# Kernel tuning notes

Hardware: AMD Instinct MI355X
Metric: run time of the kernel (lower is better)

## Reference

```python
import jax, jax.numpy as jnp
import numpy as np

EMBED_DIM = 384
NUM_HEADS = 6
HEAD_DIM = EMBED_DIM // NUM_HEADS
SCALE = HEAD_DIM ** -0.5


def setup_inputs() -> dict:
    key = jax.random.key(0)
    k1, k2 = jax.random.split(key)
    b, n, q, hw, c = 8, 5, 15, 196, EMBED_DIM
    k = 5  # shots
    x_query = jax.random.normal(k1, (b, n, q, hw, c), dtype=jnp.float32)
    x_support = jax.random.normal(k2, (b, n, k, c), dtype=jnp.float32)
    return {"x_query": x_query, "x_support": x_support}


def reference(x_query, x_support):
    b, n, k, c = x_support.shape
    _, _, q, hw, _ = x_query.shape
    h, d = NUM_HEADS, HEAD_DIM
    M = n * k            # support tokens
    P = n * q            # query images
    # support tokens as per-head queries: (b, M, h, d)
    qs = x_support.reshape(b, M, h, d)
    # query patch tokens as per-head keys/values: (b, P, hw, h, d)
    kv = x_query.reshape(b, P, hw, h, d)
    # broadcast single support-query block across all P key/value blocks
    # attn: (b, P, h, M, hw)
    attn = jnp.einsum('bmhd,bpwhd->bphmw', qs, kv) * SCALE
    attn = jax.nn.softmax(attn, axis=-1)
    # o: (b, P, M, h, d) -> (b, P, M, c)
    o_query = jnp.einsum('bphmw,bpwhd->bpmhd', attn, kv).reshape(b, P, M, c)
    o_support = x_support.reshape(b, 1, M, c)
    return (o_query, o_support)
```

## Files before the change

### kernel.cpp

```cpp
#include <hip/hip_runtime.h>
#include <stdint.h>

#define HW   196
#define CC   384
#define HH   6
#define DD   64
#define MM   25
#define PP   75
#define BB   8
#define NT   512

#define KTW  113
#define SCW  113

#define OQ_SIZE (BB * PP * MM * CC)

typedef float  f32x4 __attribute__((ext_vector_type(4)));
typedef short  s16x8 __attribute__((ext_vector_type(8)));
union Frag { uint32_t u[4]; s16x8 v; };

__device__ __forceinline__ float bflo(uint32_t u) { return __uint_as_float(u << 16); }
__device__ __forceinline__ float bfhi(uint32_t u) { return __uint_as_float(u & 0xffff0000u); }
__device__ __forceinline__ uint32_t pk_bf16(float a, float b) {
    union { __bf16 h[2]; uint32_t u; } r;
    r.h[0] = (__bf16)a; r.h[1] = (__bf16)b;
    return r.u;
}
__device__ __forceinline__ uint16_t bf16_1(float a) {
    union { __bf16 h; uint16_t u; } r; r.h = (__bf16)a; return r.u;
}

__global__ __launch_bounds__(NT, 8) void attn_kernel(
    const float* __restrict__ xq,
    const float* __restrict__ xs,
    float* __restrict__ out,
    float* __restrict__ out_sup)
{
    __shared__ uint32_t kvT[64 * KTW];
    __shared__ uint32_t scb[MM * SCW];

    const int bid  = blockIdx.x;
    const int h    = bid % HH;
    const int bp   = bid / HH;
    const int b    = bp / PP;
    const int tid  = threadIdx.x;
    const int lane = tid & 63;
    const int wv   = tid >> 6;
    const int lm   = lane & 15;
    const int quad = lane >> 4;

    if (bid < 600 && tid < 16) {
        int idx = bid * 16 + tid;
        ((float4*)out_sup)[idx * 2]     = ((const float4*)xs)[idx * 2];
        ((float4*)out_sup)[idx * 2 + 1] = ((const float4*)xs)[idx * 2 + 1];
    }

    kvT[(tid >> 3) * KTW + 104 + (tid & 7)] = 0;
    if (tid < 200) scb[(tid >> 3) * SCW + 104 + (tid & 7)] = 0;

    Frag afr[2][2];
    #pragma unroll
    for (int mt = 0; mt < 2; mt++) {
        int row = 16 * mt + lm;
        if (row >= MM) row = MM - 1;
        #pragma unroll
        for (int ks = 0; ks < 2; ks++) {
            const float* p = xs + (size_t)b * (MM * CC) + row * CC + h * DD + ks * 32 + quad * 8;
            float4 v0 = *(const float4*)p;
            float4 v1 = *(const float4*)(p + 4);
            afr[mt][ks].u[0] = pk_bf16(v0.x * 0.125f, v0.y * 0.125f);
            afr[mt][ks].u[1] = pk_bf16(v0.z * 0.125f, v0.w * 0.125f);
            afr[mt][ks].u[2] = pk_bf16(v1.x * 0.125f, v1.y * 0.125f);
            afr[mt][ks].u[3] = pk_bf16(v1.z * 0.125f, v1.w * 0.125f);
        }
    }

    {
        uint16_t* scbh = (uint16_t*)scb;
        uint16_t* kvh  = (uint16_t*)kvT;
        const float* slab = xq + (size_t)bp * (HW * CC) + h * DD;
        for (int nt = wv; nt < 13; nt += 8) {
            const int w = 16 * nt + lm;
            float4 v[2][2];
            if (w < HW) {
                const float* p = slab + (size_t)w * CC + quad * 8;
                #pragma unroll
                for (int ks = 0; ks < 2; ks++) {
                    v[ks][0] = *(const float4*)(p + ks * 32);
                    v[ks][1] = *(const float4*)(p + ks * 32 + 4);
                }
            } else {
                #pragma unroll
                for (int ks = 0; ks < 2; ks++) {
                    v[ks][0].x = v[ks][0].y = v[ks][0].z = v[ks][0].w = 0.f;
                    v[ks][1].x = v[ks][1].y = v[ks][1].z = v[ks][1].w = 0.f;
                }
            }
            Frag bf[2];
            #pragma unroll
            for (int ks = 0; ks < 2; ks++) {
                bf[ks].u[0] = pk_bf16(v[ks][0].x, v[ks][0].y);
                bf[ks].u[1] = pk_bf16(v[ks][0].z, v[ks][0].w);
                bf[ks].u[2] = pk_bf16(v[ks][1].x, v[ks][1].y);
                bf[ks].u[3] = pk_bf16(v[ks][1].z, v[ks][1].w);
            }
            f32x4 acc0 = {0.f, 0.f, 0.f, 0.f};
            f32x4 acc1 = {0.f, 0.f, 0.f, 0.f};
            #pragma unroll
            for (int ks = 0; ks < 2; ks++) {
                acc0 = __builtin_amdgcn_mfma_f32_16x16x32_bf16(afr[0][ks].v, bf[ks].v, acc0, 0, 0, 0);
                acc1 = __builtin_amdgcn_mfma_f32_16x16x32_bf16(afr[1][ks].v, bf[ks].v, acc1, 0, 0, 0);
            }
            #pragma unroll
            for (int ks = 0; ks < 2; ks++) {
                #pragma unroll
                for (int c = 0; c < 4; c++) {
                    int d = 32 * ks + 8 * quad + 2 * c;
                    kvh[d * (2 * KTW) + w]       = (uint16_t)(bf[ks].u[c] & 0xffffu);
                    kvh[(d + 1) * (2 * KTW) + w] = (uint16_t)(bf[ks].u[c] >> 16);
                }
            }
            #pragma unroll
            for (int i = 0; i < 4; i++) {
                scbh[(quad * 4 + i) * (2 * SCW) + w] = bf16_1(acc0[i]);
                int r1 = 16 + quad * 4 + i;
                if (r1 < MM) scbh[r1 * (2 * SCW) + w] = bf16_1(acc1[i]);
            }
        }
    }
    __syncthreads();

    {
        const int mt  = wv >> 2;
        const int nt2 = wv & 3;
        int arow = 16 * mt + lm;
        if (arow >= MM) arow = MM - 1;
        f32x4 acc = {0.f, 0.f, 0.f, 0.f};
        float lsum = 0.f;
        #pragma unroll
        for (int ks = 0; ks < 7; ks++) {
            Frag a, e, bfr;
            int abase = arow * SCW + ks * 16 + quad * 4;
            a.u[0] = scb[abase + 0];
            a.u[1] = scb[abase + 1];
            a.u[2] = scb[abase + 2];
            a.u[3] = scb[abase + 3];
            #pragma unroll
            for (int c = 0; c < 4; c++) {
                float e0 = __expf(bflo(a.u[c]));
                float e1 = __expf(bfhi(a.u[c]));
                lsum += e0 + e1;
                e.u[c] = pk_bf16(e0, e1);
            }
            int bbase = (16 * nt2 + lm) * KTW + ks * 16 + quad * 4;
            bfr.u[0] = kvT[bbase + 0];
            bfr.u[1] = kvT[bbase + 1];
            bfr.u[2] = kvT[bbase + 2];
            bfr.u[3] = kvT[bbase + 3];
            acc = __builtin_amdgcn_mfma_f32_16x16x32_bf16(e.v, bfr.v, acc, 0, 0, 0);
        }
        lsum -= (quad == 0) ? 4.0f : 8.0f;
        lsum += __shfl_xor(lsum, 16, 64);
        lsum += __shfl_xor(lsum, 32, 64);
        float* ob = out + (size_t)bp * (MM * CC) + h * DD + 16 * nt2 + lm;
        #pragma unroll
        for (int i = 0; i < 4; i++) {
            int m = 16 * mt + quad * 4 + i;
            float s_i = __shfl(lsum, quad * 4 + i, 64);
            float inv = __builtin_amdgcn_rcpf(s_i);
            if (m < MM) ob[(size_t)m * CC] = acc[i] * inv;
        }
    }
}

extern "C" void kernel_launch(void* const* d_in, const int* in_sizes, int n_in,
                              void* d_out, int out_size, void* d_ws, size_t ws_size,
                              hipStream_t stream) {
    const float* xq = (const float*)d_in[0];
    const float* xs = (const float*)d_in[1];
    float* out = (float*)d_out;
    float* out_sup = out + (size_t)OQ_SIZE;
    attn_kernel<<<BB * PP * HH, NT, 0, stream>>>(xq, xs, out, out_sup);
}
```

Before: 258.3 us.

## Make attention kernel persistent with double-buffered LDS and prefetched KV loads

Replaces one block per (b,p,h) tile with a persistent grid of 512 blocks, each processing a contiguous range of tiles. The next tile's K/V slab is loaded into registers while the current tile's softmax-times-V MFMA runs, and shared buffers are double-buffered so only one barrier per tile is needed. The aim is to hide global load latency behind compute and cut launch and prologue overhead. In exchange, LDS use doubles, occupancy is lowered to 4 blocks per CU, and each block works through its tiles serially, which may leave the machine underfilled.

```diff
diff --git a/kernel.cpp b/kernel.cpp
--- a/kernel.cpp
+++ b/kernel.cpp
@@ -9,6 +9,10 @@
 #define PP   75
 #define BB   8
 #define NT   512
+#define GRID 512
+#define NTILE (BB * PP * HH)
+#define QT   (NTILE / GRID)
+#define RT   (NTILE % GRID)
 
 #define KTW  113
 #define SCW  113
@@ -30,145 +34,186 @@
     union { __bf16 h; uint16_t u; } r; r.h = (__bf16)a; return r.u;
 }
 
-__global__ __launch_bounds__(NT, 8) void attn_kernel(
+__global__ __launch_bounds__(NT, 4) void attn_kernel(
     const float* __restrict__ xq,
     const float* __restrict__ xs,
     float* __restrict__ out,
     float* __restrict__ out_sup)
 {
-    __shared__ uint32_t kvT[64 * KTW];
-    __shared__ uint32_t scb[MM * SCW];
-
-    const int bid  = blockIdx.x;
-    const int h    = bid % HH;
-    const int bp   = bid / HH;
-    const int b    = bp / PP;
+    __shared__ uint32_t kvT[2][64 * KTW];
+    __shared__ uint32_t scb[2][MM * SCW];
+
+    const int blk  = blockIdx.x;
     const int tid  = threadIdx.x;
     const int lane = tid & 63;
     const int wv   = tid >> 6;
     const int lm   = lane & 15;
     const int quad = lane >> 4;
 
-    if (bid < 600 && tid < 16) {
-        int idx = bid * 16 + tid;
-        ((float4*)out_sup)[idx * 2]     = ((const float4*)xs)[idx * 2];
-        ((float4*)out_sup)[idx * 2 + 1] = ((const float4*)xs)[idx * 2 + 1];
-    }
-
-    kvT[(tid >> 3) * KTW + 104 + (tid & 7)] = 0;
-    if (tid < 200) scb[(tid >> 3) * SCW + 104 + (tid & 7)] = 0;
-
-    Frag afr[2][2];
-    #pragma unroll
-    for (int mt = 0; mt < 2; mt++) {
-        int row = 16 * mt + lm;
-        if (row >= MM) row = MM - 1;
+    {
+        int g = blk * NT + tid;
+        if (g < (BB * MM * CC) / 4)
+            ((float4*)out_sup)[g] = ((const float4*)xs)[g];
+    }
+    {
+        int r = tid >> 3, c = tid & 7;
+        kvT[0][r * KTW + 104 + c] = 0;
+        kvT[1][r * KTW + 104 + c] = 0;
+        if (tid < 200) {
+            scb[0][r * SCW + 104 + c] = 0;
+            scb[1][r * SCW + 104 + c] = 0;
+        }
+    }
+
+    const int start = blk * QT + (blk < RT ? blk : RT);
+    const int cnt   = QT + (blk < RT ? 1 : 0);
+
+    const int  w0   = 16 * wv + lm;
+    const int  w1   = 16 * (wv + 8) + lm;
+    const bool has1 = (wv < 5);
+
+    float4 kv0[4], kv1[4];
+
+    auto LOADKV = [&](float4* r, const float* slab, int w, bool act) {
+        if (act && w < HW) {
+            const float* p = slab + (size_t)w * CC + quad * 8;
+            r[0] = *(const float4*)(p);
+            r[1] = *(const float4*)(p + 4);
+            r[2] = *(const float4*)(p + 32);
+            r[3] = *(const float4*)(p + 36);
+        } else {
+            r[0] = r[1] = r[2] = r[3] = make_float4(0.f, 0.f, 0.f, 0.f);
+        }
+    };
+
+    {
+        const int bid = start;
+        const float* slab = xq + (size_t)(bid / HH) * (HW * CC) + (bid % HH) * DD;
+        LOADKV(kv0, slab, w0, true);
+        LOADKV(kv1, slab, w1, has1);
+    }
+
+    for (int i = 0; i < cnt; ++i) {
+        const int cur = i & 1;
+        const int bid = start + i;
+        const int h   = bid % HH;
+        const int bp  = bid / HH;
+        const int b   = bp / PP;
+        uint32_t* kvTc = kvT[cur];
+        uint32_t* scbc = scb[cur];
+
+        float4 ar[2][2][2];
         #pragma unroll
-        for (int ks = 0; ks < 2; ks++) {
-            const float* p = xs + (size_t)b * (MM * CC) + row * CC + h * DD + ks * 32 + quad * 8;
-            float4 v0 = *(const float4*)p;
-            float4 v1 = *(const float4*)(p + 4);
-            afr[mt][ks].u[0] = pk_bf16(v0.x * 0.125f, v0.y * 0.125f);
-            afr[mt][ks].u[1] = pk_bf16(v0.z * 0.125f, v0.w * 0.125f);
-            afr[mt][ks].u[2] = pk_bf16(v1.x * 0.125f, v1.y * 0.125f);
-            afr[mt][ks].u[3] = pk_bf16(v1.z * 0.125f, v1.w * 0.125f);
-        }
-    }
-
-    {
-        uint16_t* scbh = (uint16_t*)scb;
-        uint16_t* kvh  = (uint16_t*)kvT;
-        const float* slab = xq + (size_t)bp * (HW * CC) + h * DD;
-        for (int nt = wv; nt < 13; nt += 8) {
-            const int w = 16 * nt + lm;
-            float4 v[2][2];
-            if (w < HW) {
-                const float* p = slab + (size_t)w * CC + quad * 8;
-                #pragma unroll
-                for (int ks = 0; ks < 2; ks++) {
-                    v[ks][0] = *(const float4*)(p + ks * 32);
-                    v[ks][1] = *(const float4*)(p + ks * 32 + 4);
-                }
-            } else {
-                #pragma unroll
-                for (int ks = 0; ks < 2; ks++) {
-                    v[ks][0].x = v[ks][0].y = v[ks][0].z = v[ks][0].w = 0.f;
-                    v[ks][1].x = v[ks][1].y = v[ks][1].z = v[ks][1].w = 0.f;
-                }
-            }
-            Frag bf[2];
-            #pragma unroll
-            for (int ks = 0; ks < 2; ks++) {
-                bf[ks].u[0] = pk_bf16(v[ks][0].x, v[ks][0].y);
-                bf[ks].u[1] = pk_bf16(v[ks][0].z, v[ks][0].w);
-                bf[ks].u[2] = pk_bf16(v[ks][1].x, v[ks][1].y);
-                bf[ks].u[3] = pk_bf16(v[ks][1].z, v[ks][1].w);
-            }
+        for (int mt = 0; mt < 2; ++mt) {
+            int row = 16 * mt + lm;
+            if (row >= MM) row = MM - 1;
+            const float* p = xs + (size_t)b * (MM * CC) + row * CC + h * DD + quad * 8;
+            #pragma unroll
+            for (int ks = 0; ks < 2; ++ks) {
+                ar[mt][ks][0] = *(const float4*)(p + ks * 32);
+                ar[mt][ks][1] = *(const float4*)(p + ks * 32 + 4);
+            }
+        }
+
+        Frag b00, b01, b10, b11;
+        b00.u[0] = pk_bf16(kv0[0].x, kv0[0].y); b00.u[1] = pk_bf16(kv0[0].z, kv0[0].w);
+        b00.u[2] = pk_bf16(kv0[1].x, kv0[1].y); b00.u[3] = pk_bf16(kv0[1].z, kv0[1].w);
+        b01.u[0] = pk_bf16(kv0[2].x, kv0[2].y); b01.u[1] = pk_bf16(kv0[2].z, kv0[2].w);
+        b01.u[2] = pk_bf16(kv0[3].x, kv0[3].y); b01.u[3] = pk_bf16(kv0[3].z, kv0[3].w);
+        b10.u[0] = pk_bf16(kv1[0].x, kv1[0].y); b10.u[1] = pk_bf16(kv1[0].z, kv1[0].w);
+        b10.u[2] = pk_bf16(kv1[1].x, kv1[1].y); b10.u[3] = pk_bf16(kv1[1].z, kv1[1].w);
+        b11.u[0] = pk_bf16(kv1[2].x, kv1[2].y); b11.u[1] = pk_bf16(kv1[2].z, kv1[2].w);
+        b11.u[2] = pk_bf16(kv1[3].x, kv1[3].y); b11.u[3] = pk_bf16(kv1[3].z, kv1[3].w);
+
+        Frag afr[2][2];
+        #pragma unroll
+        for (int mt = 0; mt < 2; ++mt)
+            #pragma unroll
+            for (int ks = 0; ks < 2; ++ks) {
+                afr[mt][ks].u[0] = pk_bf16(ar[mt][ks][0].x * 0.125f, ar[mt][ks][0].y * 0.125f);
+                afr[mt][ks].u[1] = pk_bf16(ar[mt][ks][0].z * 0.125f, ar[mt][ks][0].w * 0.125f);
+                afr[mt][ks].u[2] = pk_bf16(ar[mt][ks][1].x * 0.125f, ar[mt][ks][1].y * 0.125f);
+                afr[mt][ks].u[3] = pk_bf16(ar[mt][ks][1].z * 0.125f, ar[mt][ks][1].w * 0.125f);
+            }
+
+        uint16_t* kvh = (uint16_t*)kvTc;
+        uint16_t* sch = (uint16_t*)scbc;
+
+        auto P1 = [&](const Frag& f0, const Frag& f1, int w) {
             f32x4 acc0 = {0.f, 0.f, 0.f, 0.f};
             f32x4 acc1 = {0.f, 0.f, 0.f, 0.f};
-            #pragma unroll
-            for (int ks = 0; ks < 2; ks++) {
-                acc0 = __builtin_amdgcn_mfma_f32_16x16x32_bf16(afr[0][ks].v, bf[ks].v, acc0, 0, 0, 0);
-                acc1 = __builtin_amdgcn_mfma_f32_16x16x32_bf16(afr[1][ks].v, bf[ks].v, acc1, 0, 0, 0);
-            }
-            #pragma unroll
-            for (int ks = 0; ks < 2; ks++) {
+            acc0 = __builtin_amdgcn_mfma_f32_16x16x32_bf16(afr[0][0].v, f0.v, acc0, 0, 0, 0);
+            acc1 = __builtin_amdgcn_mfma_f32_16x16x32_bf16(afr[1][0].v, f0.v, acc1, 0, 0, 0);
+            acc0 = __builtin_amdgcn_mfma_f32_16x16x32_bf16(afr[0][1].v, f1.v, acc0, 0, 0, 0);
+            acc1 = __builtin_amdgcn_mfma_f32_16x16x32_bf16(afr[1][1].v, f1.v, acc1, 0, 0, 0);
+            #pragma unroll
+            for (int c = 0; c < 4; ++c) {
+                int d0 = 8 * quad + 2 * c;
+                kvh[d0 * (2 * KTW) + w]          = (uint16_t)(f0.u[c] & 0xffffu);
+                kvh[(d0 + 1) * (2 * KTW) + w]    = (uint16_t)(f0.u[c] >> 16);
+                kvh[(32 + d0) * (2 * KTW) + w]   = (uint16_t)(f1.u[c] & 0xffffu);
+                kvh[(33 + d0) * (2 * KTW) + w]   = (uint16_t)(f1.u[c] >> 16);
+            }
+            #pragma unroll
+            for (int ii = 0; ii < 4; ++ii) {
+                sch[(quad * 4 + ii) * (2 * SCW) + w] = bf16_1(acc0[ii]);
+                int r1 = 16 + quad * 4 + ii;
+                if (r1 < MM) sch[r1 * (2 * SCW) + w] = bf16_1(acc1[ii]);
+            }
+        };
+        P1(b00, b01, w0);
+        if (has1) P1(b10, b11, w1);
+
+        __syncthreads();
+
+        if (i + 1 < cnt) {
+            const int bid2 = bid + 1;
+            const float* slab = xq + (size_t)(bid2 / HH) * (HW * CC) + (bid2 % HH) * DD;
+            LOADKV(kv0, slab, w0, true);
+            LOADKV(kv1, slab, w1, has1);
+        }
+        __builtin_amdgcn_sched_barrier(0);
+
+        {
+            const int mt  = wv >> 2;
+            const int nt2 = wv & 3;
+            int arow = 16 * mt + lm;
+            if (arow >= MM) arow = MM - 1;
+            f32x4 acc = {0.f, 0.f, 0.f, 0.f};
+            float lsum = 0.f;
+            #pragma unroll
+            for (int ks = 0; ks < 7; ++ks) {
+                Frag a, e, bfr;
+                int abase = arow * SCW + ks * 16 + quad * 4;
+                a.u[0] = scbc[abase + 0];
+                a.u[1] = scbc[abase + 1];
+                a.u[2] = scbc[abase + 2];
+                a.u[3] = scbc[abase + 3];
                 #pragma unroll
-                for (int c = 0; c < 4; c++) {
-                    int d = 32 * ks + 8 * quad + 2 * c;
-                    kvh[d * (2 * KTW) + w]       = (uint16_t)(bf[ks].u[c] & 0xffffu);
-                    kvh[(d + 1) * (2 * KTW) + w] = (uint16_t)(bf[ks].u[c] >> 16);
+                for (int c = 0; c < 4; ++c) {
+                    float e0 = __expf(bflo(a.u[c]));
+                    float e1 = __expf(bfhi(a.u[c]));
+                    lsum += e0 + e1;
+                    e.u[c] = pk_bf16(e0, e1);
                 }
-            }
-            #pragma unroll
-            for (int i = 0; i < 4; i++) {
-                scbh[(quad * 4 + i) * (2 * SCW) + w] = bf16_1(acc0[i]);
-                int r1 = 16 + quad * 4 + i;
-                if (r1 < MM) scbh[r1 * (2 * SCW) + w] = bf16_1(acc1[i]);
-            }
-        }
-    }
-    __syncthreads();
-
-    {
-        const int mt  = wv >> 2;
-        const int nt2 = wv & 3;
-        int arow = 16 * mt + lm;
-        if (arow >= MM) arow = MM - 1;
-        f32x4 acc = {0.f, 0.f, 0.f, 0.f};
-        float lsum = 0.f;
-        #pragma unroll
-        for (int ks = 0; ks < 7; ks++) {
-            Frag a, e, bfr;
-            int abase = arow * SCW + ks * 16 + quad * 4;
-            a.u[0] = scb[abase + 0];
-            a.u[1] = scb[abase + 1];
-            a.u[2] = scb[abase + 2];
-            a.u[3] = scb[abase + 3];
-            #pragma unroll
-            for (int c = 0; c < 4; c++) {
-                float e0 = __expf(bflo(a.u[c]));
-                float e1 = __expf(bfhi(a.u[c]));
-                lsum += e0 + e1;
-                e.u[c] = pk_bf16(e0, e1);
-            }
-            int bbase = (16 * nt2 + lm) * KTW + ks * 16 + quad * 4;
-            bfr.u[0] = kvT[bbase + 0];
-            bfr.u[1] = kvT[bbase + 1];
-            bfr.u[2] = kvT[bbase + 2];
-            bfr.u[3] = kvT[bbase + 3];
-            acc = __builtin_amdgcn_mfma_f32_16x16x32_bf16(e.v, bfr.v, acc, 0, 0, 0);
-        }
-        lsum -= (quad == 0) ? 4.0f : 8.0f;
-        lsum += __shfl_xor(lsum, 16, 64);
-        lsum += __shfl_xor(lsum, 32, 64);
-        float* ob = out + (size_t)bp * (MM * CC) + h * DD + 16 * nt2 + lm;
-        #pragma unroll
-        for (int i = 0; i < 4; i++) {
-            int m = 16 * mt + quad * 4 + i;
-            float s_i = __shfl(lsum, quad * 4 + i, 64);
-            float inv = __builtin_amdgcn_rcpf(s_i);
-            if (m < MM) ob[(size_t)m * CC] = acc[i] * inv;
+                int bbase = (16 * nt2 + lm) * KTW + ks * 16 + quad * 4;
+                bfr.u[0] = kvTc[bbase + 0];
+                bfr.u[1] = kvTc[bbase + 1];
+                bfr.u[2] = kvTc[bbase + 2];
+                bfr.u[3] = kvTc[bbase + 3];
+                acc = __builtin_amdgcn_mfma_f32_16x16x32_bf16(e.v, bfr.v, acc, 0, 0, 0);
+            }
+            lsum -= (quad == 0) ? 4.0f : 8.0f;
+            lsum += __shfl_xor(lsum, 16, 64);
+            lsum += __shfl_xor(lsum, 32, 64);
+            float* ob = out + (size_t)bp * (MM * CC) + h * DD + 16 * nt2 + lm;
+            #pragma unroll
+            for (int ii = 0; ii < 4; ++ii) {
+                int m = 16 * mt + quad * 4 + ii;
+                float s_i = __shfl(lsum, quad * 4 + ii, 64);
+                float inv = __builtin_amdgcn_rcpf(s_i);
+                if (m < MM) ob[(size_t)m * CC] = acc[ii] * inv;
+            }
         }
     }
 }
@@ -180,5 +225,5 @@
     const float* xs = (const float*)d_in[1];
     float* out = (float*)d_out;
     float* out_sup = out + (size_t)OQ_SIZE;
-    attn_kernel<<<BB * PP * HH, NT, 0, stream>>>(xq, xs, out, out_sup);
-}
+    attn_kernel<<<GRID, NT, 0, stream>>>(xq, xs, out, out_sup);
+}
```

After: 268.3 us. +3.9%, slower.
